# Kernel optimization log

Hardware: AMD Instinct MI355X
Metric: run time of the kernel (lower is better)

## Reference

```python
import jax, jax.numpy as jnp
import numpy as np

T, B, C, U = 4000, 64, 64, 200
NEG_INF = jnp.float32(-1e30)


def setup_inputs() -> dict:
    key = jax.random.key(0)
    k1, k2 = jax.random.split(key)
    inputs = jax.random.normal(k1, (T, B, C), dtype=jnp.float32)  # time-major logits
    targets = jax.random.randint(k2, (B, U), 0, C, dtype=jnp.int32)
    return {"inputs": inputs, "targets": targets}


def reference(inputs, targets):
    # Transducer.forward: transitions is None -> log_softmax over classes.
    log_probs = jax.nn.log_softmax(inputs, axis=-1)  # [T, B, C]
    # emit[t, b, u] = log_probs[t, b, targets[b, u]]
    b_idx = jnp.arange(B)[:, None]  # [B, 1]
    emit = log_probs[:, b_idx, targets]  # [T, B, U]

    # ASG-style monotone alignment forward DP (no blank, repeats collapse):
    # alpha[t, u] = emit[t, u] + logsumexp(alpha[t-1, u], alpha[t-1, u-1])
    alpha0 = jnp.full((B, U), NEG_INF, dtype=inputs.dtype).at[:, 0].set(emit[0, :, 0])

    def step(alpha, emit_t):
        shifted = jnp.concatenate(
            [jnp.full((B, 1), NEG_INF, dtype=alpha.dtype), alpha[:, :-1]], axis=1
        )
        return emit_t + jnp.logaddexp(alpha, shifted), None

    alpha_T, _ = jax.lax.scan(step, alpha0, emit[1:])  # scan over T-1 frames
    losses = -alpha_T[:, U - 1]  # negated forward score per sample
    return jnp.mean(losses)  # TransducerLossFunction returns torch.mean(loss)
```

## Files before the change

### kernel.cpp

```cpp
#include <hip/hip_runtime.h>

#define T_DIM 4000
#define B_DIM 64
#define C_DIM 64
#define U_DIM 200
#define LOG2E 1.4426950408889634f
#define LN2 0.6931471805599453f

#define PAIRS 2000
#define PB_BYTES (PAIRS * 800)
#define NSLOT 20

__device__ __forceinline__ float hw_exp2(float x) { return __builtin_amdgcn_exp2f(x); }
__device__ __forceinline__ float hw_log2(float x) { return __builtin_amdgcn_logf(x); }

template <int CTRL>
__device__ __forceinline__ int dpp_i(int x) {
    return __builtin_amdgcn_update_dpp(0, x, CTRL, 0xF, 0xF, true);
}
template <int CTRL>
__device__ __forceinline__ float dpp_f(float x) {
    return __uint_as_float((unsigned)dpp_i<CTRL>((int)__float_as_uint(x)));
}

__device__ __forceinline__ unsigned rne_bf16(float v) {
    unsigned b = __float_as_uint(v);
    return b + 0x7FFFu + ((b >> 16) & 1u);
}

__global__ __launch_bounds__(256) void prep_kernel(const float* __restrict__ in,
                                                   const int* __restrict__ tgt,
                                                   unsigned* __restrict__ eg,
                                                   float* __restrict__ out) {
    __shared__ float ex[16 * 8 * 68];
    __shared__ unsigned tgc[400];
    __shared__ float red[4];
    const int tid = threadIdx.x;
    const int bg = blockIdx.x & 7;
    const int tc = blockIdx.x >> 3;
    const int t0 = tc * 16, b0 = bg * 8;

    for (int o = tid; o < 400; o += 256) {
        int4 tv = ((const int4*)tgt)[bg * 400 + o];
        tgc[o] = (unsigned)(tv.x & 63) | ((unsigned)(tv.y & 63) << 8)
               | ((unsigned)(tv.z & 63) << 16) | ((unsigned)(tv.w & 63) << 24);
    }
    #pragma unroll
    for (int k = 0; k < 8; ++k) {
        int flat = k * 256 + tid;
        int t_l = flat >> 7, i = flat & 127, b_l = i >> 4, q = i & 15;
        float4 v = *(const float4*)(in + (size_t)(t0 + t_l) * 4096 + (b0 + b_l) * 64 + q * 4);
        float4 e;
        e.x = hw_exp2(v.x * LOG2E); e.y = hw_exp2(v.y * LOG2E);
        e.z = hw_exp2(v.z * LOG2E); e.w = hw_exp2(v.w * LOG2E);
        *(float4*)&ex[(t_l * 8 + b_l) * 68 + q * 4] = e;
    }
    __syncthreads();

    {
        float v = 0.0f;
        if (tid < 128) {
            const float4* p = (const float4*)&ex[tid * 68];
            float s = 0.0f;
            #pragma unroll
            for (int j = 0; j < 16; ++j) { float4 a = p[j]; s += (a.x + a.y) + (a.z + a.w); }
            v = hw_log2(s);
        }
        #pragma unroll
        for (int o = 32; o > 0; o >>= 1) v += __shfl_xor(v, o);
        if ((tid & 63) == 0) red[tid >> 6] = v;
    }

    for (int it = 0; it < 13; ++it) {
        int o = it * 256 + tid;
        if (o < 3200) {
            int l = o % 50;
            int rest = o / 50;
            int b_l = rest & 7, tp_l = rest >> 3;
            unsigned tw = tgc[b_l * 50 + l];
            int c0 = tw & 255, c1 = (tw >> 8) & 255, c2 = (tw >> 16) & 255, c3 = tw >> 24;
            const float* plo = &ex[(tp_l * 16 + b_l) * 68];
            const float* phi = plo + 8 * 68;
            uint4 w;
            w.x = (rne_bf16(plo[c0]) >> 16) | (rne_bf16(plo[c1]) & 0xFFFF0000u);
            w.y = (rne_bf16(plo[c2]) >> 16) | (rne_bf16(plo[c3]) & 0xFFFF0000u);
            w.z = (rne_bf16(phi[c0]) >> 16) | (rne_bf16(phi[c1]) & 0xFFFF0000u);
            w.w = (rne_bf16(phi[c2]) >> 16) | (rne_bf16(phi[c3]) & 0xFFFF0000u);
            *(uint4*)((char*)eg + (size_t)(b0 + b_l) * PB_BYTES
                      + (size_t)(tc * 8 + tp_l) * 800 + l * 16) = w;
        }
    }
    __syncthreads();
    if (tid == 0)
        atomicAdd(out, (red[0] + red[1] + red[2] + red[3]) * (LN2 / 64.0f));
}

struct ScanState { float A0, A1, A2, A3; int S, D; };

__device__ __forceinline__ void renorm(ScanState& st, int lane) {
    float m = fmaxf(fmaxf(st.A0, st.A1), fmaxf(st.A2, st.A3));
    int e = (int)((__float_as_uint(m) >> 23) & 0xFFu);
    int cand = st.S + e - 127;
    int snb = dpp_i<0x138>(st.S);
    if (lane == 0) snb = -(1 << 28);
    int snew = max(cand, snb);
    int k = st.S - snew;
    st.A0 = ldexpf(st.A0, k);
    st.A1 = ldexpf(st.A1, k);
    st.A2 = ldexpf(st.A2, k);
    st.A3 = ldexpf(st.A3, k);
    st.S = snew;
    st.D = min(dpp_i<0x138>(snew) - snew, 60);
}

__device__ __forceinline__ void step(ScanState& st, float e0, float e1, float e2, float e3) {
    float sh = ldexpf(dpp_f<0x138>(st.A3), st.D);
    sh = fminf(sh, 1.125899906842624e15f);
    float t0 = st.A0 + sh;
    float t1 = st.A1 + st.A0;
    float t2 = st.A2 + st.A1;
    float t3 = st.A3 + st.A2;
    st.A0 = e0 * t0; st.A1 = e1 * t1; st.A2 = e2 * t2; st.A3 = e3 * t3;
}

__device__ __forceinline__ void brenorm(ScanState& st) {
    float m = fmaxf(fmaxf(st.A0, st.A1), fmaxf(st.A2, st.A3));
    int e = (int)((__float_as_uint(m) >> 23) & 0xFFu);
    int cand = st.S + e - 127;
    int snb = dpp_i<0x130>(st.S);
    int snew = max(cand, snb);
    int k = st.S - snew;
    st.A0 = ldexpf(st.A0, k);
    st.A1 = ldexpf(st.A1, k);
    st.A2 = ldexpf(st.A2, k);
    st.A3 = ldexpf(st.A3, k);
    st.S = snew;
    st.D = min(dpp_i<0x130>(snew) - snew, 60);
}

__device__ __forceinline__ void bstep(ScanState& st, float e0, float e1, float e2, float e3) {
    float e4s = fminf(ldexpf(dpp_f<0x130>(e0), st.D), 1.125899906842624e15f);
    float b0n = dpp_f<0x130>(st.A0);
    float g0 = e0 * st.A0, g1 = e1 * st.A1, g2 = e2 * st.A2, g3 = e3 * st.A3;
    st.A0 = g0 + g1; st.A1 = g1 + g2; st.A2 = g2 + g3; st.A3 = g3 + e4s * b0n;
}

__device__ __forceinline__ ScanState scan_init(const float* in, const int* tgt, int lane, int b) {
    float v0 = in[b * 64 + (tgt[b * U_DIM] & 63)];
    ScanState st;
    st.A0 = (lane == 0) ? hw_exp2(v0 * LOG2E) : 0.0f;
    st.A1 = 0.0f; st.A2 = 0.0f; st.A3 = 0.0f;
    st.S = 0; st.D = 0;
    return st;
}

#define LO(x) __uint_as_float((x) << 16)
#define HI(x) __uint_as_float((x) & 0xFFFF0000u)

__global__ __launch_bounds__(128, 1) void scan2_kernel(const float* __restrict__ in,
                                                       const int* __restrict__ tgt,
                                                       const unsigned* __restrict__ eg,
                                                       float* __restrict__ out) {
    __shared__ float jb0[64], jb1[64], jb2[64], jb3[64];
    __shared__ int jsb[64];
    const int lane = threadIdx.x & 63;
    const int wv = threadIdx.x >> 6;
    const int b = blockIdx.x;
    const int lidx = (lane < 50) ? lane : 49;
    const char* egb = (const char*)eg + (size_t)b * PB_BYTES;

    ScanState st;
    if (wv == 1) {
        st.A0 = 0.0f; st.A1 = 0.0f; st.A2 = 0.0f;
        st.A3 = (lane == 49) ? 1.0f : 0.0f;
        st.S = 0; st.D = 0;
        int off = 1999 * 800 + lidx * 16;
        uint4 wb[NSLOT];
        #pragma unroll
        for (int j = 0; j < NSLOT; ++j) { wb[j] = *(const uint4*)(egb + off); off -= 800; }
        for (int k = 0; k < 49; ++k) {
            #pragma unroll
            for (int j = 0; j < NSLOT; ++j) {
                if ((j & 3) == 0) brenorm(st);
                uint4 w = wb[j];
                wb[j] = *(const uint4*)(egb + off); off -= 800;
                bstep(st, LO(w.z), HI(w.z), LO(w.w), HI(w.w));
                bstep(st, LO(w.x), HI(w.x), LO(w.y), HI(w.y));
            }
        }
        #pragma unroll
        for (int j = 0; j < NSLOT; ++j) {
            if ((j & 3) == 0) brenorm(st);
            uint4 w = wb[j];
            bstep(st, LO(w.z), HI(w.z), LO(w.w), HI(w.w));
            if (j < NSLOT - 1) bstep(st, LO(w.x), HI(w.x), LO(w.y), HI(w.y));
        }
        brenorm(st);
        jb0[lane] = st.A0; jb1[lane] = st.A1; jb2[lane] = st.A2; jb3[lane] = st.A3;
        jsb[lane] = st.S;
    } else {
        st = scan_init(in, tgt, lane, b);
        int off = 800 + lidx * 16;
        uint4 wb[NSLOT];
        #pragma unroll
        for (int j = 0; j < NSLOT; ++j) { wb[j] = *(const uint4*)(egb + off); off += 800; }
        uint2 h0 = *(const uint2*)(egb + lidx * 16 + 8);
        step(st, LO(h0.x), HI(h0.x), LO(h0.y), HI(h0.y));
        for (int k = 0; k < 49; ++k) {
            #pragma unroll
            for (int j = 0; j < NSLOT; ++j) {
                if ((j & 3) == 0) renorm(st, lane);
                uint4 w = wb[j];
                wb[j] = *(const uint4*)(egb + off); off += 800;
                step(st, LO(w.x), HI(w.x), LO(w.y), HI(w.y));
                step(st, LO(w.z), HI(w.z), LO(w.w), HI(w.w));
            }
        }
        #pragma unroll
        for (int j = 0; j < NSLOT; ++j) {
            if ((j & 3) == 0) renorm(st, lane);
            uint4 w = wb[j];
            step(st, LO(w.x), HI(w.x), LO(w.y), HI(w.y));
            if (j < NSLOT - 1) step(st, LO(w.z), HI(w.z), LO(w.w), HI(w.w));
        }
        renorm(st, lane);
    }
    __syncthreads();
    if (wv == 0) {
        float d = st.A0 * jb0[lane] + st.A1 * jb1[lane]
                + st.A2 * jb2[lane] + st.A3 * jb3[lane];
        float ll = (lane < 50) ? hw_log2(fmaxf(d, 1e-38f)) + (float)(st.S + jsb[lane])
                               : -1e30f;
        float mx = ll;
        #pragma unroll
        for (int o = 32; o > 0; o >>= 1) mx = fmaxf(mx, __shfl_xor(mx, o));
        float s = (lane < 50) ? hw_exp2(ll - mx) : 0.0f;
        #pragma unroll
        for (int o = 32; o > 0; o >>= 1) s += __shfl_xor(s, o);
        if (lane == 0) atomicAdd(out, -(mx + hw_log2(s)) * (LN2 / 64.0f));
    }
}

__global__ __launch_bounds__(256) void lse_sum_kernel(const float* __restrict__ in,
                                                      float* __restrict__ out) {
    const int lane = threadIdx.x & 63;
    const int w = threadIdx.x >> 6;
    const int wid = blockIdx.x * 4 + w;
    const int ROWS = (T_DIM * B_DIM) / 1024;
    const float* p = in + (size_t)wid * ROWS * 64 + lane;
    float acc = 0.0f;
    for (int i = 0; i < ROWS; i += 2) {
        float xa = p[(size_t)i * 64];
        float xb = p[(size_t)(i + 1) * 64];
        float ea = hw_exp2(xa * LOG2E);
        float eb = hw_exp2(xb * LOG2E);
        #pragma unroll
        for (int off = 32; off > 0; off >>= 1) {
            ea += __shfl_xor(ea, off);
            eb += __shfl_xor(eb, off);
        }
        acc += hw_log2(ea) + hw_log2(eb);
    }
    __shared__ float red[4];
    if (lane == 0) red[w] = acc;
    __syncthreads();
    if (threadIdx.x == 0)
        atomicAdd(out, (red[0] + red[1] + red[2] + red[3]) * (LN2 / 64.0f));
}

__global__ __launch_bounds__(64) void scan_fb(const float* __restrict__ in,
                                              const int* __restrict__ tgt,
                                              float* __restrict__ out) {
    const int lane = threadIdx.x;
    const int b = blockIdx.x;
    const int lidx = (lane < 50) ? lane : 49;
    int4 tg = ((const int4*)(tgt + b * U_DIM))[lidx];
    tg.x &= 63; tg.y &= 63; tg.z &= 63; tg.w &= 63;
    ScanState st = scan_init(in, tgt, lane, b);
    const char* inb = (const char*)in;
    int o0 = 16384 + b * 256 + tg.x * 4;
    int o1 = 16384 + b * 256 + tg.y * 4;
    int o2 = 16384 + b * 256 + tg.z * 4;
    int o3 = 16384 + b * 256 + tg.w * 4;
    const int m0 = 3999 * 16384 + b * 256 + tg.x * 4;
    const int m1 = m0 + (tg.y - tg.x) * 4;
    const int m2 = m0 + (tg.z - tg.x) * 4;
    const int m3 = m0 + (tg.w - tg.x) * 4;
    float f0[16], f1[16], f2[16], f3[16];
    #pragma unroll
    for (int j = 0; j < 16; ++j) {
        f0[j] = *(const float*)(inb + min(o0, m0)); o0 += 16384;
        f1[j] = *(const float*)(inb + min(o1, m1)); o1 += 16384;
        f2[j] = *(const float*)(inb + min(o2, m2)); o2 += 16384;
        f3[j] = *(const float*)(inb + min(o3, m3)); o3 += 16384;
    }
    for (int k = 0; k < 249; ++k) {
        #pragma unroll
        for (int j = 0; j < 16; ++j) {
            if (j == 0 || j == 8) renorm(st, lane);
            float e0 = hw_exp2(f0[j] * LOG2E);
            float e1 = hw_exp2(f1[j] * LOG2E);
            float e2 = hw_exp2(f2[j] * LOG2E);
            float e3 = hw_exp2(f3[j] * LOG2E);
            f0[j] = *(const float*)(inb + min(o0, m0)); o0 += 16384;
            f1[j] = *(const float*)(inb + min(o1, m1)); o1 += 16384;
            f2[j] = *(const float*)(inb + min(o2, m2)); o2 += 16384;
            f3[j] = *(const float*)(inb + min(o3, m3)); o3 += 16384;
            step(st, e0, e1, e2, e3);
        }
    }
    #pragma unroll
    for (int j = 0; j < 15; ++j) {
        if (j == 0 || j == 8) renorm(st, lane);
        float e0 = hw_exp2(f0[j] * LOG2E);
        float e1 = hw_exp2(f1[j] * LOG2E);
        float e2 = hw_exp2(f2[j] * LOG2E);
        float e3 = hw_exp2(f3[j] * LOG2E);
        step(st, e0, e1, e2, e3);
    }
    if (lane == 49) {
        float a2 = hw_log2(fmaxf(st.A3, 1e-38f)) + (float)st.S;
        atomicAdd(out, -a2 * (LN2 / 64.0f));
    }
}

extern "C" void kernel_launch(void* const* d_in, const int* in_sizes, int n_in,
                              void* d_out, int out_size, void* d_ws, size_t ws_size,
                              hipStream_t stream) {
    const float* inputs = (const float*)d_in[0];
    const int* targets = (const int*)d_in[1];
    float* out = (float*)d_out;

    (void)hipMemsetAsync(out, 0, sizeof(float), stream);

    const size_t eg_bytes = (size_t)B_DIM * PB_BYTES;
    if (ws_size >= eg_bytes) {
        unsigned* eg = (unsigned*)d_ws;
        prep_kernel<<<2000, 256, 0, stream>>>(inputs, targets, eg, out);
        scan2_kernel<<<B_DIM, 128, 0, stream>>>(inputs, targets, eg, out);
    } else {
        scan_fb<<<B_DIM, 64, 0, stream>>>(inputs, targets, out);
        lse_sum_kernel<<<256, 256, 0, stream>>>(inputs, out);
    }
}
```

Before: 189.0 us.

## Fuse prep and scan kernels with bitmask-signalled producer/consumer overlap

Merges the emission-prep kernel and the scan kernel into one launch. The first 64 blocks run the forward and backward scans and the remaining 2000 blocks produce bf16 emission chunks, ordered from both ends of time. Producers set per-batch-group ready bits with release atomics, and the scan waves spin on those bits before reading each chunk, so the scans can start before all prep work has finished. The scan state also keeps the neighbour shift as a float multiplier instead of an exponent, turning an ldexp into a multiply in the step. This relies on the scan blocks being co-resident with the producer blocks, adds atomic polling, and adds a memset for the bitmask.

```diff
diff --git a/kernel.cpp b/kernel.cpp
--- a/kernel.cpp
+++ b/kernel.cpp
@@ -10,6 +10,8 @@
 #define PAIRS 2000
 #define PB_BYTES (PAIRS * 800)
 #define NSLOT 20
+#define EG_BYTES ((size_t)B_DIM * PB_BYTES)
+#define BM_WORDS (8 * 4)
 
 __device__ __forceinline__ float hw_exp2(float x) { return __builtin_amdgcn_exp2f(x); }
 __device__ __forceinline__ float hw_log2(float x) { return __builtin_amdgcn_logf(x); }
@@ -27,75 +29,11 @@
     unsigned b = __float_as_uint(v);
     return b + 0x7FFFu + ((b >> 16) & 1u);
 }
-
-__global__ __launch_bounds__(256) void prep_kernel(const float* __restrict__ in,
-                                                   const int* __restrict__ tgt,
-                                                   unsigned* __restrict__ eg,
-                                                   float* __restrict__ out) {
-    __shared__ float ex[16 * 8 * 68];
-    __shared__ unsigned tgc[400];
-    __shared__ float red[4];
-    const int tid = threadIdx.x;
-    const int bg = blockIdx.x & 7;
-    const int tc = blockIdx.x >> 3;
-    const int t0 = tc * 16, b0 = bg * 8;
-
-    for (int o = tid; o < 400; o += 256) {
-        int4 tv = ((const int4*)tgt)[bg * 400 + o];
-        tgc[o] = (unsigned)(tv.x & 63) | ((unsigned)(tv.y & 63) << 8)
-               | ((unsigned)(tv.z & 63) << 16) | ((unsigned)(tv.w & 63) << 24);
-    }
-    #pragma unroll
-    for (int k = 0; k < 8; ++k) {
-        int flat = k * 256 + tid;
-        int t_l = flat >> 7, i = flat & 127, b_l = i >> 4, q = i & 15;
-        float4 v = *(const float4*)(in + (size_t)(t0 + t_l) * 4096 + (b0 + b_l) * 64 + q * 4);
-        float4 e;
-        e.x = hw_exp2(v.x * LOG2E); e.y = hw_exp2(v.y * LOG2E);
-        e.z = hw_exp2(v.z * LOG2E); e.w = hw_exp2(v.w * LOG2E);
-        *(float4*)&ex[(t_l * 8 + b_l) * 68 + q * 4] = e;
-    }
-    __syncthreads();
-
-    {
-        float v = 0.0f;
-        if (tid < 128) {
-            const float4* p = (const float4*)&ex[tid * 68];
-            float s = 0.0f;
-            #pragma unroll
-            for (int j = 0; j < 16; ++j) { float4 a = p[j]; s += (a.x + a.y) + (a.z + a.w); }
-            v = hw_log2(s);
-        }
-        #pragma unroll
-        for (int o = 32; o > 0; o >>= 1) v += __shfl_xor(v, o);
-        if ((tid & 63) == 0) red[tid >> 6] = v;
-    }
-
-    for (int it = 0; it < 13; ++it) {
-        int o = it * 256 + tid;
-        if (o < 3200) {
-            int l = o % 50;
-            int rest = o / 50;
-            int b_l = rest & 7, tp_l = rest >> 3;
-            unsigned tw = tgc[b_l * 50 + l];
-            int c0 = tw & 255, c1 = (tw >> 8) & 255, c2 = (tw >> 16) & 255, c3 = tw >> 24;
-            const float* plo = &ex[(tp_l * 16 + b_l) * 68];
-            const float* phi = plo + 8 * 68;
-            uint4 w;
-            w.x = (rne_bf16(plo[c0]) >> 16) | (rne_bf16(plo[c1]) & 0xFFFF0000u);
-            w.y = (rne_bf16(plo[c2]) >> 16) | (rne_bf16(plo[c3]) & 0xFFFF0000u);
-            w.z = (rne_bf16(phi[c0]) >> 16) | (rne_bf16(phi[c1]) & 0xFFFF0000u);
-            w.w = (rne_bf16(phi[c2]) >> 16) | (rne_bf16(phi[c3]) & 0xFFFF0000u);
-            *(uint4*)((char*)eg + (size_t)(b0 + b_l) * PB_BYTES
-                      + (size_t)(tc * 8 + tp_l) * 800 + l * 16) = w;
-        }
-    }
-    __syncthreads();
-    if (tid == 0)
-        atomicAdd(out, (red[0] + red[1] + red[2] + red[3]) * (LN2 / 64.0f));
-}
-
-struct ScanState { float A0, A1, A2, A3; int S, D; };
+__device__ __forceinline__ unsigned pk_bf16(float lo, float hi) {
+    return (rne_bf16(lo) >> 16) | (rne_bf16(hi) & 0xFFFF0000u);
+}
+
+struct ScanState { float A0, A1, A2, A3, F; int S; };
 
 __device__ __forceinline__ void renorm(ScanState& st, int lane) {
     float m = fmaxf(fmaxf(st.A0, st.A1), fmaxf(st.A2, st.A3));
@@ -110,12 +48,11 @@
     st.A2 = ldexpf(st.A2, k);
     st.A3 = ldexpf(st.A3, k);
     st.S = snew;
-    st.D = min(dpp_i<0x138>(snew) - snew, 60);
+    st.F = ldexpf(1.0f, min(dpp_i<0x138>(snew) - snew, 60));
 }
 
 __device__ __forceinline__ void step(ScanState& st, float e0, float e1, float e2, float e3) {
-    float sh = ldexpf(dpp_f<0x138>(st.A3), st.D);
-    sh = fminf(sh, 1.125899906842624e15f);
+    float sh = fminf(dpp_f<0x138>(st.A3) * st.F, 1.125899906842624e15f);
     float t0 = st.A0 + sh;
     float t1 = st.A1 + st.A0;
     float t2 = st.A2 + st.A1;
@@ -135,11 +72,11 @@
     st.A2 = ldexpf(st.A2, k);
     st.A3 = ldexpf(st.A3, k);
     st.S = snew;
-    st.D = min(dpp_i<0x130>(snew) - snew, 60);
+    st.F = ldexpf(1.0f, min(dpp_i<0x130>(snew) - snew, 60));
 }
 
 __device__ __forceinline__ void bstep(ScanState& st, float e0, float e1, float e2, float e3) {
-    float e4s = fminf(ldexpf(dpp_f<0x130>(e0), st.D), 1.125899906842624e15f);
+    float e4s = fminf(dpp_f<0x130>(e0) * st.F, 1.125899906842624e15f);
     float b0n = dpp_f<0x130>(st.A0);
     float g0 = e0 * st.A0, g1 = e1 * st.A1, g2 = e2 * st.A2, g3 = e3 * st.A3;
     st.A0 = g0 + g1; st.A1 = g1 + g2; st.A2 = g2 + g3; st.A3 = g3 + e4s * b0n;
@@ -150,94 +87,206 @@
     ScanState st;
     st.A0 = (lane == 0) ? hw_exp2(v0 * LOG2E) : 0.0f;
     st.A1 = 0.0f; st.A2 = 0.0f; st.A3 = 0.0f;
-    st.S = 0; st.D = 0;
+    st.S = 0; st.F = 1.0f;
     return st;
 }
 
 #define LO(x) __uint_as_float((x) << 16)
 #define HI(x) __uint_as_float((x) & 0xFFFF0000u)
 
-__global__ __launch_bounds__(128, 1) void scan2_kernel(const float* __restrict__ in,
+__global__ __launch_bounds__(256, 1) void fused_kernel(const float* __restrict__ in,
                                                        const int* __restrict__ tgt,
-                                                       const unsigned* __restrict__ eg,
+                                                       unsigned* __restrict__ eg,
+                                                       unsigned long long* __restrict__ bm,
                                                        float* __restrict__ out) {
+    __shared__ float ex[16 * 8 * 68];
+    __shared__ unsigned tgc[400];
+    __shared__ float red[4];
     __shared__ float jb0[64], jb1[64], jb2[64], jb3[64];
     __shared__ int jsb[64];
-    const int lane = threadIdx.x & 63;
-    const int wv = threadIdx.x >> 6;
-    const int b = blockIdx.x;
-    const int lidx = (lane < 50) ? lane : 49;
-    const char* egb = (const char*)eg + (size_t)b * PB_BYTES;
-
-    ScanState st;
-    if (wv == 1) {
-        st.A0 = 0.0f; st.A1 = 0.0f; st.A2 = 0.0f;
-        st.A3 = (lane == 49) ? 1.0f : 0.0f;
-        st.S = 0; st.D = 0;
-        int off = 1999 * 800 + lidx * 16;
-        uint4 wb[NSLOT];
-        #pragma unroll
-        for (int j = 0; j < NSLOT; ++j) { wb[j] = *(const uint4*)(egb + off); off -= 800; }
-        for (int k = 0; k < 49; ++k) {
+
+    if (blockIdx.x < 64) {
+        const int wv = threadIdx.x >> 6;
+        if (wv >= 2) { __syncthreads(); return; }
+        const int lane = threadIdx.x & 63;
+        const int b = blockIdx.x;
+        const int lidx = (lane < 50) ? lane : 49;
+        const char* egb = (const char*)eg + (size_t)b * PB_BYTES;
+        const unsigned long long* bmg = bm + (b >> 3) * 4;
+
+        ScanState st;
+        if (wv == 1) {
+            st.A0 = 0.0f; st.A1 = 0.0f; st.A2 = 0.0f;
+            st.A3 = (lane == 49) ? 1.0f : 0.0f;
+            st.S = 0; st.F = 1.0f;
+            int lowB = 250;
+            int off = 1999 * 800 + lidx * 16;
+            uint4 wb[NSLOT];
+            while (lowB > 247) {
+                int ch = lowB - 1;
+                unsigned long long v = __hip_atomic_load(&bmg[ch >> 6], __ATOMIC_ACQUIRE,
+                                                         __HIP_MEMORY_SCOPE_AGENT);
+                unsigned long long inv = ~(v << (63 - (ch & 63)));
+                int add = inv ? __builtin_clzll(inv) : ((ch & 63) + 1);
+                if (!add) __builtin_amdgcn_s_sleep(1);
+                lowB -= add;
+            }
+            #pragma unroll
+            for (int j = 0; j < NSLOT; ++j) { wb[j] = *(const uint4*)(egb + off); off -= 800; }
+            for (int k = 0; k < 49; ++k) {
+                int need = (1960 - 20 * k) >> 3;
+                while (lowB > need) {
+                    int ch = lowB - 1;
+                    unsigned long long v = __hip_atomic_load(&bmg[ch >> 6], __ATOMIC_ACQUIRE,
+                                                             __HIP_MEMORY_SCOPE_AGENT);
+                    unsigned long long inv = ~(v << (63 - (ch & 63)));
+                    int add = inv ? __builtin_clzll(inv) : ((ch & 63) + 1);
+                    if (!add) __builtin_amdgcn_s_sleep(1);
+                    lowB -= add;
+                }
+                #pragma unroll
+                for (int j = 0; j < NSLOT; ++j) {
+                    if ((j & 3) == 0) brenorm(st);
+                    uint4 w = wb[j];
+                    wb[j] = *(const uint4*)(egb + off); off -= 800;
+                    bstep(st, LO(w.z), HI(w.z), LO(w.w), HI(w.w));
+                    bstep(st, LO(w.x), HI(w.x), LO(w.y), HI(w.y));
+                }
+            }
             #pragma unroll
             for (int j = 0; j < NSLOT; ++j) {
                 if ((j & 3) == 0) brenorm(st);
                 uint4 w = wb[j];
-                wb[j] = *(const uint4*)(egb + off); off -= 800;
                 bstep(st, LO(w.z), HI(w.z), LO(w.w), HI(w.w));
-                bstep(st, LO(w.x), HI(w.x), LO(w.y), HI(w.y));
-            }
-        }
-        #pragma unroll
-        for (int j = 0; j < NSLOT; ++j) {
-            if ((j & 3) == 0) brenorm(st);
-            uint4 w = wb[j];
-            bstep(st, LO(w.z), HI(w.z), LO(w.w), HI(w.w));
-            if (j < NSLOT - 1) bstep(st, LO(w.x), HI(w.x), LO(w.y), HI(w.y));
-        }
-        brenorm(st);
-        jb0[lane] = st.A0; jb1[lane] = st.A1; jb2[lane] = st.A2; jb3[lane] = st.A3;
-        jsb[lane] = st.S;
-    } else {
-        st = scan_init(in, tgt, lane, b);
-        int off = 800 + lidx * 16;
-        uint4 wb[NSLOT];
-        #pragma unroll
-        for (int j = 0; j < NSLOT; ++j) { wb[j] = *(const uint4*)(egb + off); off += 800; }
-        uint2 h0 = *(const uint2*)(egb + lidx * 16 + 8);
-        step(st, LO(h0.x), HI(h0.x), LO(h0.y), HI(h0.y));
-        for (int k = 0; k < 49; ++k) {
+                if (j < NSLOT - 1) bstep(st, LO(w.x), HI(w.x), LO(w.y), HI(w.y));
+            }
+            brenorm(st);
+            jb0[lane] = st.A0; jb1[lane] = st.A1; jb2[lane] = st.A2; jb3[lane] = st.A3;
+            jsb[lane] = st.S;
+            __syncthreads();
+        } else {
+            st = scan_init(in, tgt, lane, b);
+            int readyF = 0;
+            int off = 800 + lidx * 16;
+            uint4 wb[NSLOT];
+            while (readyF <= 2) {
+                unsigned long long v = __hip_atomic_load(&bmg[readyF >> 6], __ATOMIC_ACQUIRE,
+                                                         __HIP_MEMORY_SCOPE_AGENT);
+                unsigned long long inv = ~(v >> (readyF & 63));
+                int add = inv ? __builtin_ctzll(inv) : (64 - (readyF & 63));
+                if (!add) __builtin_amdgcn_s_sleep(1);
+                readyF += add;
+            }
+            #pragma unroll
+            for (int j = 0; j < NSLOT; ++j) { wb[j] = *(const uint4*)(egb + off); off += 800; }
+            uint2 h0 = *(const uint2*)(egb + lidx * 16 + 8);
+            step(st, LO(h0.x), HI(h0.x), LO(h0.y), HI(h0.y));
+            for (int k = 0; k < 49; ++k) {
+                int need = (40 + 20 * k) >> 3;
+                while (readyF <= need) {
+                    unsigned long long v = __hip_atomic_load(&bmg[readyF >> 6], __ATOMIC_ACQUIRE,
+                                                             __HIP_MEMORY_SCOPE_AGENT);
+                    unsigned long long inv = ~(v >> (readyF & 63));
+                    int add = inv ? __builtin_ctzll(inv) : (64 - (readyF & 63));
+                    if (!add) __builtin_amdgcn_s_sleep(1);
+                    readyF += add;
+                }
+                #pragma unroll
+                for (int j = 0; j < NSLOT; ++j) {
+                    if ((j & 3) == 0) renorm(st, lane);
+                    uint4 w = wb[j];
+                    wb[j] = *(const uint4*)(egb + off); off += 800;
+                    step(st, LO(w.x), HI(w.x), LO(w.y), HI(w.y));
+                    step(st, LO(w.z), HI(w.z), LO(w.w), HI(w.w));
+                }
+            }
             #pragma unroll
             for (int j = 0; j < NSLOT; ++j) {
                 if ((j & 3) == 0) renorm(st, lane);
                 uint4 w = wb[j];
-                wb[j] = *(const uint4*)(egb + off); off += 800;
                 step(st, LO(w.x), HI(w.x), LO(w.y), HI(w.y));
-                step(st, LO(w.z), HI(w.z), LO(w.w), HI(w.w));
-            }
+                if (j < NSLOT - 1) step(st, LO(w.z), HI(w.z), LO(w.w), HI(w.w));
+            }
+            renorm(st, lane);
+            __syncthreads();
+            float d = st.A0 * jb0[lane] + st.A1 * jb1[lane]
+                    + st.A2 * jb2[lane] + st.A3 * jb3[lane];
+            float ll = (lane < 50) ? hw_log2(fmaxf(d, 1e-38f)) + (float)(st.S + jsb[lane])
+                                   : -1e30f;
+            float mx = ll;
+            #pragma unroll
+            for (int o = 32; o > 0; o >>= 1) mx = fmaxf(mx, __shfl_xor(mx, o));
+            float s = (lane < 50) ? hw_exp2(ll - mx) : 0.0f;
+            #pragma unroll
+            for (int o = 32; o > 0; o >>= 1) s += __shfl_xor(s, o);
+            if (lane == 0) atomicAdd(out, -(mx + hw_log2(s)) * (LN2 / 64.0f));
+        }
+        return;
+    }
+
+    const int tid = threadIdx.x;
+    const int id = blockIdx.x - 64;
+    const int bg = id & 7;
+    const int jj = id >> 3;
+    const int tc = (jj & 1) ? (249 - (jj >> 1)) : (jj >> 1);
+    const int t0 = tc * 16, b0 = bg * 8;
+
+    for (int o = tid; o < 400; o += 256) {
+        int4 tv = ((const int4*)tgt)[bg * 400 + o];
+        tgc[o] = (unsigned)(tv.x & 63) | ((unsigned)(tv.y & 63) << 8)
+               | ((unsigned)(tv.z & 63) << 16) | ((unsigned)(tv.w & 63) << 24);
+    }
+    #pragma unroll
+    for (int k = 0; k < 8; ++k) {
+        int flat = k * 256 + tid;
+        int t_l = flat >> 7, i = flat & 127, b_l = i >> 4, q = i & 15;
+        float4 v = *(const float4*)(in + (size_t)(t0 + t_l) * 4096 + (b0 + b_l) * 64 + q * 4);
+        float4 e;
+        e.x = hw_exp2(v.x * LOG2E); e.y = hw_exp2(v.y * LOG2E);
+        e.z = hw_exp2(v.z * LOG2E); e.w = hw_exp2(v.w * LOG2E);
+        *(float4*)&ex[(t_l * 8 + b_l) * 68 + q * 4] = e;
+    }
+    __syncthreads();
+
+    {
+        float v = 0.0f;
+        if (tid < 128) {
+            const float4* p = (const float4*)&ex[tid * 68];
+            float s = 0.0f;
+            #pragma unroll
+            for (int j = 0; j < 16; ++j) { float4 a = p[j]; s += (a.x + a.y) + (a.z + a.w); }
+            v = hw_log2(s);
         }
         #pragma unroll
-        for (int j = 0; j < NSLOT; ++j) {
-            if ((j & 3) == 0) renorm(st, lane);
-            uint4 w = wb[j];
-            step(st, LO(w.x), HI(w.x), LO(w.y), HI(w.y));
-            if (j < NSLOT - 1) step(st, LO(w.z), HI(w.z), LO(w.w), HI(w.w));
-        }
-        renorm(st, lane);
+        for (int o = 32; o > 0; o >>= 1) v += __shfl_xor(v, o);
+        if ((tid & 63) == 0) red[tid >> 6] = v;
+    }
+
+    for (int it = 0; it < 13; ++it) {
+        int o = it * 256 + tid;
+        if (o < 3200) {
+            int l = o % 50;
+            int rest = o / 50;
+            int b_l = rest & 7, tp_l = rest >> 3;
+            unsigned tw = tgc[b_l * 50 + l];
+            int c0 = tw & 255, c1 = (tw >> 8) & 255, c2 = (tw >> 16) & 255, c3 = tw >> 24;
+            const float* plo = &ex[(tp_l * 16 + b_l) * 68];
+            const float* phi = plo + 8 * 68;
+            uint4 w;
+            w.x = pk_bf16(plo[c0], plo[c1]);
+            w.y = pk_bf16(plo[c2], plo[c3]);
+            w.z = pk_bf16(phi[c0], phi[c1]);
+            w.w = pk_bf16(phi[c2], phi[c3]);
+            *(uint4*)((char*)eg + (size_t)(b0 + b_l) * PB_BYTES
+                      + (size_t)(tc * 8 + tp_l) * 800 + l * 16) = w;
+        }
     }
     __syncthreads();
-    if (wv == 0) {
-        float d = st.A0 * jb0[lane] + st.A1 * jb1[lane]
-                + st.A2 * jb2[lane] + st.A3 * jb3[lane];
-        float ll = (lane < 50) ? hw_log2(fmaxf(d, 1e-38f)) + (float)(st.S + jsb[lane])
-                               : -1e30f;
-        float mx = ll;
-        #pragma unroll
-        for (int o = 32; o > 0; o >>= 1) mx = fmaxf(mx, __shfl_xor(mx, o));
-        float s = (lane < 50) ? hw_exp2(ll - mx) : 0.0f;
-        #pragma unroll
-        for (int o = 32; o > 0; o >>= 1) s += __shfl_xor(s, o);
-        if (lane == 0) atomicAdd(out, -(mx + hw_log2(s)) * (LN2 / 64.0f));
+    if (tid == 0) {
+        atomicAdd(out, (red[0] + red[1] + red[2] + red[3]) * (LN2 / 64.0f));
+        __threadfence();
+        __hip_atomic_fetch_or(&bm[bg * 4 + (tc >> 6)], 1ULL << (tc & 63),
+                              __ATOMIC_RELEASE, __HIP_MEMORY_SCOPE_AGENT);
     }
 }
 
@@ -333,11 +382,11 @@
 
     (void)hipMemsetAsync(out, 0, sizeof(float), stream);
 
-    const size_t eg_bytes = (size_t)B_DIM * PB_BYTES;
-    if (ws_size >= eg_bytes) {
+    if (ws_size >= EG_BYTES + BM_WORDS * sizeof(unsigned long long)) {
         unsigned* eg = (unsigned*)d_ws;
-        prep_kernel<<<2000, 256, 0, stream>>>(inputs, targets, eg, out);
-        scan2_kernel<<<B_DIM, 128, 0, stream>>>(inputs, targets, eg, out);
+        unsigned long long* bmp = (unsigned long long*)((char*)d_ws + EG_BYTES);
+        (void)hipMemsetAsync(bmp, 0, BM_WORDS * sizeof(unsigned long long), stream);
+        fused_kernel<<<64 + 2000, 256, 0, stream>>>(inputs, targets, eg, bmp, out);
     } else {
         scan_fb<<<B_DIM, 64, 0, stream>>>(inputs, targets, out);
         lse_sum_kernel<<<256, 256, 0, stream>>>(inputs, out);
```

Measured after the change: 332.6 us. 76.0% more time.
